# Kernel optimization log

Measured on AMD Instinct MI355X. Metric: run time of the kernel, lower is better.

Reference implementation:

```python
import jax, jax.numpy as jnp
import numpy as np

H, P, G, NS, K = 8, 64, 64, 64, 3          # heads, dim_head, slice_num, d_state, d_conv
D_INNER = H * P                            # 512
CONV_DIM = D_INNER + 2 * NS                # 640
D_IN_PROJ = 2 * D_INNER + 2 * NS + 2 * H   # 1168


def setup_inputs() -> dict:
    key = jax.random.key(0)
    ks = jax.random.split(key, 10)
    dim, Bsz, N = 256, 4, 8192
    s = 0.02
    return {
        "x": jax.random.normal(ks[0], (Bsz, N, dim), jnp.float32),
        "W_fx": jax.random.normal(ks[1], (D_INNER, dim), jnp.float32) * s,
        "b_fx": jnp.zeros((D_INNER,), jnp.float32),
        "W_x": jax.random.normal(ks[2], (D_INNER, dim), jnp.float32) * s,
        "b_x": jnp.zeros((D_INNER,), jnp.float32),
        "W_slice": jax.random.normal(ks[3], (G, P), jnp.float32) * s,
        "b_slice": jnp.zeros((G,), jnp.float32),
        "temperature": jnp.full((1, H, 1, 1), 0.5, jnp.float32),
        "hy_in_w": jax.random.normal(ks[4], (D_IN_PROJ, D_INNER), jnp.float32) * s,
        "hy_conv_w": jax.random.normal(ks[5], (CONV_DIM, K), jnp.float32) * s,
        "hy_conv_b": jnp.zeros((CONV_DIM,), jnp.float32),
        "hy_dt_bias": jnp.log(jnp.expm1(jnp.full((H,), 0.01, jnp.float32))),
        "hy_A_log": jnp.log(jnp.linspace(1.0, 16.0, H)).astype(jnp.float32),
        "hy_D": jnp.ones((H,), jnp.float32),
        "hy_fcD_w": jax.random.normal(ks[6], (H, D_INNER), jnp.float32) * s,
        "hy_norm_w": jnp.ones((D_INNER,), jnp.float32),
        "hy_out_w": jax.random.normal(ks[7], (D_INNER, D_INNER), jnp.float32) * s,
        "out_w": jax.random.normal(ks[8], (dim, D_INNER), jnp.float32) * s,
        "out_b": jnp.zeros((dim,), jnp.float32),
    }


def _hydra(u, in_w, conv_w, conv_b, dt_bias, A_log, Dp, fcD_w, norm_w, out_w):
    # Bidirectional Mamba2-style selective scan (Hydra, non mem-eff path).
    Bt, L, _ = u.shape
    zxbcdt = u @ in_w.T                                   # (B, L, 1168)
    z = zxbcdt[..., :D_INNER]
    xBC = zxbcdt[..., D_INNER:D_INNER + CONV_DIM]
    dt = zxbcdt[..., -2 * H:]
    # fwd dts for fwd copies, time-flipped bwd dts stacked along batch
    dt = jnp.concatenate([dt[..., :H], jnp.flip(dt[..., H:], axis=1)], axis=0)
    dt = jax.nn.softplus(dt + dt_bias)                    # (2B, L, H)
    # depthwise causal conv, kernel K, left pad K-1 then silu
    xp = jnp.pad(xBC, ((0, 0), (K - 1, 0), (0, 0)))
    xBC = sum(xp[:, k:k + L, :] * conv_w[:, k] for k in range(K)) + conv_b
    xBC = jax.nn.silu(xBC)
    x = xBC[..., :D_INNER]
    Bm = xBC[..., D_INNER:D_INNER + NS]
    Cm = xBC[..., D_INNER + NS:]
    x_og = x
    x2 = jnp.concatenate([x, jnp.flip(x, 1)], 0).reshape(2 * Bt, L, H, P)
    B2 = jnp.concatenate([Bm, jnp.flip(Bm, 1)], 0)        # (2B, L, NS)
    C2 = jnp.concatenate([Cm, jnp.flip(Cm, 1)], 0)
    dA = jnp.exp(dt * (-jnp.exp(A_log)))                  # (2B, L, H)
    dBx = jnp.einsum('blh,bln,blhp->blhpn', dt, B2, x2)   # (2B, L, H, P, NS)

    def step(h, inp):
        dA_t, dBx_t, C_t = inp
        h = h * dA_t[:, :, None, None] + dBx_t
        return h, jnp.einsum('bhpn,bn->bhp', h, C_t)

    h0 = jnp.zeros((2 * Bt, H, P, NS), u.dtype)
    _, ys = jax.lax.scan(step, h0, (dA.transpose(1, 0, 2), dBx.transpose(1, 0, 2, 3, 4), C2.transpose(1, 0, 2)))
    y = ys.transpose(1, 0, 2, 3).reshape(2 * Bt, L, D_INNER)
    y_fw, y_bw = y[:Bt], jnp.flip(y[Bt:], 1)
    # quasiseparable: strictly-lower (shift fwd) + strictly-upper (shift bwd) + diagonal
    y = jnp.pad(y_fw[:, :-1], ((0, 0), (1, 0), (0, 0))) + jnp.pad(y_bw[:, 1:], ((0, 0), (0, 1), (0, 0)))
    y = y + x_og * jnp.repeat(x_og @ fcD_w.T + Dp, P, axis=-1)
    # gated RMSNorm (gate before norm), then out projection
    yg = y * jax.nn.silu(z)
    yg = yg * jax.lax.rsqrt(jnp.mean(jnp.square(yg), -1, keepdims=True) + 1e-5) * norm_w
    return yg @ out_w.T


def reference(x, W_fx, b_fx, W_x, b_x, W_slice, b_slice, temperature,
              hy_in_w, hy_conv_w, hy_conv_b, hy_dt_bias, hy_A_log, hy_D,
              hy_fcD_w, hy_norm_w, hy_out_w, out_w, out_b):
    B, N, _ = x.shape
    fx = (x @ W_fx.T + b_fx).reshape(B, N, H, P).transpose(0, 2, 1, 3)   # (B,H,N,P)
    xm = (x @ W_x.T + b_x).reshape(B, N, H, P).transpose(0, 2, 1, 3)
    temp = jnp.maximum(temperature, 1e-6)
    sw = jax.nn.softmax((xm @ W_slice.T + b_slice) / temp, axis=-1)      # (B,H,N,G)
    snorm = sw.sum(2)                                                     # (B,H,G)
    st = jnp.einsum('bhnc,bhng->bhgc', fx, sw) / (snorm + 1e-5)[..., None]
    st = st.transpose(0, 2, 1, 3).reshape(B, G, D_INNER)                  # (B,G,512)
    ot = _hydra(st, hy_in_w, hy_conv_w, hy_conv_b, hy_dt_bias, hy_A_log, hy_D,
                hy_fcD_w, hy_norm_w, hy_out_w)
    ot = ot.reshape(B, G, H, P).transpose(0, 2, 1, 3)                     # (B,H,G,P)
    out = jnp.einsum('bhgc,bhng->bhnc', ot, sw).transpose(0, 2, 1, 3).reshape(B, N, D_INNER)
    return out @ out_w.T + out_b
```

## Files before the change

kernel.cpp:

```cpp
#include <hip/hip_runtime.h>
#include <hip/hip_bf16.h>
#include <cstdint>
#include <cstddef>

#define Hh 8
#define DIN 512
#define CONVD 640
#define DPROJ 1168
#define NTOK 8192
#define DIM 256

typedef __attribute__((ext_vector_type(8))) short short8;
typedef __attribute__((ext_vector_type(4))) float f32x4;

static __device__ __forceinline__ float sigmoidf_(float x) { return 1.f / (1.f + expf(-x)); }
static __device__ __forceinline__ unsigned short f2b(float f) {
  __hip_bfloat16 h = __float2bfloat16(f);
  return *(unsigned short*)&h;
}
static __device__ __forceinline__ float b2f(unsigned short u) {
  union { unsigned int i; float f; } cv; cv.i = ((unsigned int)u) << 16; return cv.f;
}
static __device__ __forceinline__ void gll16(const void* g, void* l) {
  __builtin_amdgcn_global_load_lds((const __attribute__((address_space(1))) void*)g,
                                   (__attribute__((address_space(3))) void*)l, 16, 0, 0);
}

__global__ __launch_bounds__(256) void k_cvt(
    const float* __restrict__ wfx, const float* __restrict__ wx, const float* __restrict__ outw,
    const float* __restrict__ inw, const float* __restrict__ how,
    const float* __restrict__ bfx, const float* __restrict__ bx,
    const float* __restrict__ x,
    unsigned short* __restrict__ wcat, unsigned short* __restrict__ outwb,
    unsigned short* __restrict__ inwb, unsigned short* __restrict__ howb,
    float* __restrict__ bcat, unsigned short* __restrict__ xb) {
  const int blk = blockIdx.x;
  if (blk < 4096) {
    const int e = (blk * 256 + threadIdx.x) * 8;
    float4 v0 = *(const float4*)(x + e);
    float4 v1 = *(const float4*)(x + e + 4);
    short8 o;
    o[0] = (short)f2b(v0.x); o[1] = (short)f2b(v0.y);
    o[2] = (short)f2b(v0.z); o[3] = (short)f2b(v0.w);
    o[4] = (short)f2b(v1.x); o[5] = (short)f2b(v1.y);
    o[6] = (short)f2b(v1.z); o[7] = (short)f2b(v1.w);
    *(short8*)(xb + e) = o;
    return;
  }
  const int e = ((blk - 4096) * 256 + threadIdx.x) * 4;
  if (e >= 1253376) {
    const int i = e - 1253376;
    float4 v;
    if (i < 512) v = *(const float4*)(bfx + i);
    else         v = *(const float4*)(bx + (i - 512));
    *(float4*)(bcat + i) = v;
    return;
  }
  const float* src; unsigned short* dst; int i;
  if (e < 131072)        { i = e;           src = wfx;  dst = wcat; }
  else if (e < 262144)   { i = e - 131072;  src = wx;   dst = wcat + 131072; }
  else if (e < 393216)   { i = e - 262144;  src = outw; dst = outwb; }
  else if (e < 991232)   { i = e - 393216;  src = inw;  dst = inwb; }
  else                   { i = e - 991232;  src = how;  dst = howb; }
  float4 v = *(const float4*)(src + i);
  ushort4 o;
  o.x = f2b(v.x); o.y = f2b(v.y); o.z = f2b(v.z); o.w = f2b(v.w);
  *(ushort4*)(dst + i) = o;
}

__global__ __launch_bounds__(256) void k_front(
    const unsigned short* __restrict__ xb, const unsigned short* __restrict__ wcat,
    const float* __restrict__ bcat, const float* __restrict__ Wslice,
    const float* __restrict__ bslice, const float* __restrict__ temperature,
    unsigned short* __restrict__ cb, unsigned short* __restrict__ swb) {
  __shared__ unsigned short lds[32768];
  const int tid = threadIdx.x;
  const int m0 = blockIdx.x * 128;
  const int n0 = blockIdx.y * 128;
  const int w = tid >> 6, lane = tid & 63;
  const int l15 = lane & 15, kq = lane >> 4;
  const int wm = (w & 1) * 64, wn = (w >> 1) * 64;
  float bs[4];
#pragma unroll
  for (int j = 0; j < 4; ++j) bs[j] = bcat[n0 + wn + j * 16 + l15];
  f32x4 acc[4][4];
#pragma unroll
  for (int i = 0; i < 4; ++i)
#pragma unroll
    for (int j = 0; j < 4; ++j) acc[i][j] = (f32x4){0.f, 0.f, 0.f, 0.f};

  auto stage = [&](int buf, int kt) {
    unsigned short* As = lds + buf * 8192;
    unsigned short* Bs = lds + 16384 + buf * 8192;
#pragma unroll
    for (int i = 0; i < 4; ++i) {
      const int c = tid + 256 * i;
      const int m = c >> 3, kb = c & 7;
      const int kbs = (kb ^ (m & 7)) * 8;
      gll16(&xb[(size_t)(m0 + m) * 256 + kt + kbs], &As[c * 8]);
      gll16(&wcat[(size_t)(n0 + m) * 256 + kt + kbs], &Bs[c * 8]);
    }
  };

  stage(0, 0);
  __syncthreads();
  int buf = 0;
  for (int t = 0; t < 4; ++t) {
    if (t < 3) stage(buf ^ 1, (t + 1) * 64);
    const unsigned short* As = lds + buf * 8192;
    const unsigned short* Bs = lds + 16384 + buf * 8192;
#pragma unroll
    for (int kw = 0; kw < 2; ++kw) {
      short8 af[4], bfr[4];
#pragma unroll
      for (int i = 0; i < 4; ++i) {
        const int rm = wm + i * 16 + l15;
        af[i]  = *(const short8*)&As[rm * 64 + ((kw * 32 + kq * 8) ^ ((rm & 7) << 3))];
        const int rn = wn + i * 16 + l15;
        bfr[i] = *(const short8*)&Bs[rn * 64 + ((kw * 32 + kq * 8) ^ ((rn & 7) << 3))];
      }
#pragma unroll
      for (int i = 0; i < 4; ++i)
#pragma unroll
        for (int j = 0; j < 4; ++j)
          acc[i][j] = __builtin_amdgcn_mfma_f32_16x16x32_bf16(af[i], bfr[j], acc[i][j], 0, 0, 0);
    }
    __syncthreads();
    buf ^= 1;
  }
  unsigned short* Cs = lds;
#pragma unroll
  for (int i = 0; i < 4; ++i)
#pragma unroll
    for (int j = 0; j < 4; ++j)
#pragma unroll
      for (int r = 0; r < 4; ++r) {
        const int m = wm + i * 16 + kq * 4 + r;
        const int n = wn + j * 16 + l15;
        Cs[m * 136 + n] = f2b(acc[i][j][r] + bs[j]);
      }
  __syncthreads();
  if (blockIdx.y < 4) {
#pragma unroll
    for (int it = 0; it < 8; ++it) {
      const int c = tid + 256 * it;
      const int m = c >> 4, seg = c & 15;
      *(short8*)&cb[(size_t)(m0 + m) * 512 + n0 + seg * 8] = *(const short8*)&Cs[m * 136 + seg * 8];
    }
    return;
  }
  const int h0 = (n0 - 512) >> 6;
  const int bidx = m0 >> 13, nb = m0 & (NTOK - 1);
  short8 sbfr[2][4];
#pragma unroll
  for (int kt = 0; kt < 2; ++kt)
#pragma unroll
    for (int j = 0; j < 4; ++j) {
      const float* wp = Wslice + (j * 16 + l15) * 64 + kt * 32 + kq * 8;
      short8 t;
#pragma unroll
      for (int u = 0; u < 8; ++u) t[u] = (short)f2b(wp[u]);
      sbfr[kt][j] = t;
    }
  float sbs[4];
#pragma unroll
  for (int j = 0; j < 4; ++j) sbs[j] = bslice[j * 16 + l15];
  f32x4 sacc[2][2][4];
#pragma unroll
  for (int hl = 0; hl < 2; ++hl)
#pragma unroll
    for (int i = 0; i < 2; ++i)
#pragma unroll
      for (int j = 0; j < 4; ++j) sacc[hl][i][j] = (f32x4){0.f, 0.f, 0.f, 0.f};
#pragma unroll
  for (int hl = 0; hl < 2; ++hl)
#pragma unroll
    for (int kt = 0; kt < 2; ++kt) {
      short8 af[2];
#pragma unroll
      for (int i = 0; i < 2; ++i)
        af[i] = *(const short8*)&Cs[(w * 32 + i * 16 + l15) * 136 + hl * 64 + kt * 32 + kq * 8];
#pragma unroll
      for (int i = 0; i < 2; ++i)
#pragma unroll
        for (int j = 0; j < 4; ++j)
          sacc[hl][i][j] = __builtin_amdgcn_mfma_f32_16x16x32_bf16(af[i], sbfr[kt][j], sacc[hl][i][j], 0, 0, 0);
    }
  __syncthreads();
#pragma unroll
  for (int hl = 0; hl < 2; ++hl) {
    const float invt = 1.f / fmaxf(temperature[h0 + hl], 1e-6f);
#pragma unroll
    for (int i = 0; i < 2; ++i)
#pragma unroll
      for (int r = 0; r < 4; ++r) {
        float v[4];
        float m = -1e30f;
#pragma unroll
        for (int j = 0; j < 4; ++j) { v[j] = (sacc[hl][i][j][r] + sbs[j]) * invt; m = fmaxf(m, v[j]); }
#pragma unroll
        for (int off = 8; off; off >>= 1) m = fmaxf(m, __shfl_xor(m, off));
        float s = 0.f;
#pragma unroll
        for (int j = 0; j < 4; ++j) { v[j] = expf(v[j] - m); s += v[j]; }
#pragma unroll
        for (int off = 8; off; off >>= 1) s += __shfl_xor(s, off);
        const float inv = 1.f / s;
        const int row = w * 32 + i * 16 + kq * 4 + r;
#pragma unroll
        for (int j = 0; j < 4; ++j) Cs[row * 136 + hl * 64 + j * 16 + l15] = f2b(v[j] * inv);
      }
  }
  __syncthreads();
#pragma unroll
  for (int it = 0; it < 8; ++it) {
    const int c = tid + 256 * it;
    const int head = c >> 10, row = (c >> 3) & 127, seg = c & 7;
    *(short8*)&swb[((size_t)(bidx * 8 + h0 + head) * NTOK + nb + row) * 64 + seg * 8] =
        *(const short8*)&Cs[row * 136 + head * 64 + seg * 8];
  }
}

__global__ __launch_bounds__(256) void k_st(
    const unsigned short* __restrict__ swb, const unsigned short* __restrict__ cb,
    float* __restrict__ st_part, float* __restrict__ sn_part) {
  __shared__ unsigned short swT[64][136];
  __shared__ unsigned short fxT[64][136];
  const int tid = threadIdx.x;
  const int bh = blockIdx.y;
  const int b = bh >> 3, h = bh & 7;
  const int nbase = blockIdx.x * 512;
  const int w = tid >> 6, lane = tid & 63;
  const int l15 = lane & 15, kq = lane >> 4;
  short8 ones;
#pragma unroll
  for (int u = 0; u < 8; ++u) ones[u] = (short)0x3F80;
  f32x4 acc[4], accO[4];
#pragma unroll
  for (int i = 0; i < 4; ++i) {
    acc[i] = (f32x4){0.f, 0.f, 0.f, 0.f};
    accO[i] = (f32x4){0.f, 0.f, 0.f, 0.f};
  }
  for (int nc = 0; nc < 4; ++nc) {
    const int n0 = nbase + nc * 128;
#pragma unroll
    for (int i = 0; i < 4; ++i) {
      const int c = tid + 256 * i, n = c >> 3, gc = c & 7;
      short8 sv = *(const short8*)&swb[((size_t)bh * NTOK + n0 + n) * 64 + gc * 8];
      short8 fv = *(const short8*)&cb[((size_t)(b * NTOK) + n0 + n) * 512 + h * 64 + gc * 8];
      const int csw = n ^ (gc << 4);
#pragma unroll
      for (int u = 0; u < 8; ++u) {
        swT[gc * 8 + u][csw] = (unsigned short)sv[u];
        fxT[gc * 8 + u][csw] = (unsigned short)fv[u];
      }
    }
    __syncthreads();
#pragma unroll
    for (int kw = 0; kw < 4; ++kw) {
      const int brow = w * 16 + l15;
      const short8 bfr = *(const short8*)&fxT[brow][(kw * 32 + kq * 8) ^ ((brow >> 3) << 4)];
#pragma unroll
      for (int mi = 0; mi < 4; ++mi) {
        const int arow = mi * 16 + l15;
        const short8 af = *(const short8*)&swT[arow][(kw * 32 + kq * 8) ^ ((arow >> 3) << 4)];
        acc[mi] = __builtin_amdgcn_mfma_f32_16x16x32_bf16(af, bfr, acc[mi], 0, 0, 0);
        if (w == 0)
          accO[mi] = __builtin_amdgcn_mfma_f32_16x16x32_bf16(af, ones, accO[mi], 0, 0, 0);
      }
    }
    __syncthreads();
  }
  float* stp = st_part + ((size_t)blockIdx.x * 32 + bh) * 4096;
#pragma unroll
  for (int mi = 0; mi < 4; ++mi)
#pragma unroll
    for (int r = 0; r < 4; ++r)
      stp[(mi * 16 + kq * 4 + r) * 64 + w * 16 + l15] = acc[mi][r];
  if (w == 0 && l15 == 0) {
    float* snp = sn_part + ((size_t)blockIdx.x * 32 + bh) * 64;
#pragma unroll
    for (int mi = 0; mi < 4; ++mi)
#pragma unroll
      for (int r = 0; r < 4; ++r)
        snp[mi * 16 + kq * 4 + r] = accO[mi][r];
  }
}

__global__ __launch_bounds__(256) void k_stnorm(
    const float* __restrict__ st_part, const float* __restrict__ sn_part,
    unsigned short* __restrict__ st2b) {
  const int idx = blockIdx.x * 256 + threadIdx.x;
  const int p = idx & 63, g = (idx >> 6) & 63, h = (idx >> 12) & 7, b = idx >> 15;
  const int bh = idx >> 12;
  const int gp = idx & 4095;
  float s = 0.f, sn = 0.f;
#pragma unroll
  for (int bx = 0; bx < 16; ++bx) {
    s  += st_part[((size_t)bx * 32 + bh) * 4096 + gp];
    sn += sn_part[((size_t)bx * 32 + bh) * 64 + g];
  }
  const float v = s / (sn + 1e-5f);
  st2b[(size_t)(b * 64 + g) * DIN + h * 64 + p] = f2b(v);
}

__global__ __launch_bounds__(256) void k_inproj(
    const unsigned short* __restrict__ st2b, const unsigned short* __restrict__ inwb,
    float* __restrict__ zx) {
  const int tid = threadIdx.x;
  const int m0 = blockIdx.x * 64;
  const int n0 = blockIdx.y * 64;
  const int w = tid >> 6, lane = tid & 63;
  const int l15 = lane & 15, kq = lane >> 4;
  f32x4 acc[4];
#pragma unroll
  for (int j = 0; j < 4; ++j) acc[j] = (f32x4){0.f, 0.f, 0.f, 0.f};
  const int arow = m0 + w * 16 + l15;
#pragma unroll
  for (int kc = 0; kc < 16; ++kc) {
    const short8 af = *(const short8*)&st2b[(size_t)arow * DIN + kc * 32 + kq * 8];
#pragma unroll
    for (int j = 0; j < 4; ++j) {
      int brow = n0 + j * 16 + l15;
      if (brow >= DPROJ) brow = 0;
      const short8 bfr = *(const short8*)&inwb[(size_t)brow * DIN + kc * 32 + kq * 8];
      acc[j] = __builtin_amdgcn_mfma_f32_16x16x32_bf16(af, bfr, acc[j], 0, 0, 0);
    }
  }
#pragma unroll
  for (int j = 0; j < 4; ++j)
#pragma unroll
    for (int r = 0; r < 4; ++r) {
      const int m = m0 + w * 16 + kq * 4 + r;
      const int c = n0 + j * 16 + l15;
      if (c < DPROJ) zx[(size_t)m * DPROJ + c] = acc[j][r];
    }
}

__global__ __launch_bounds__(256) void k_prep(
    const float* __restrict__ zx, const float* __restrict__ convw, const float* __restrict__ convb,
    const float* __restrict__ dtbias, const float* __restrict__ Alog,
    float* __restrict__ xbc, float* __restrict__ dt2, float* __restrict__ ldA2) {
  const int idx = blockIdx.x * 256 + threadIdx.x;
  const int NCONV = 4 * 64 * CONVD;
  if (idx < NCONV) {
    const int c = idx % CONVD;
    const int l = (idx / CONVD) & 63;
    const int b = idx / (CONVD * 64);
    float acc = convb[c];
#pragma unroll
    for (int k = 0; k < 3; ++k) {
      const int ls = l - 2 + k;
      if (ls >= 0) acc += zx[(size_t)(b * 64 + ls) * DPROJ + DIN + c] * convw[c * 3 + k];
    }
    xbc[idx] = acc * sigmoidf_(acc);
  } else if (idx < NCONV + 8 * 64 * 8) {
    const int j = idx - NCONV;
    const int h = j & 7, l = (j >> 3) & 63, bb = j >> 9;
    float raw;
    if (bb < 4) raw = zx[(size_t)(bb * 64 + l) * DPROJ + 1152 + h];
    else        raw = zx[(size_t)((bb - 4) * 64 + (63 - l)) * DPROJ + 1160 + h];
    const float d = raw + dtbias[h];
    const float sp = (d > 20.f) ? d : log1pf(expf(d));
    dt2[j] = sp;
    ldA2[j] = sp * -expf(Alog[h]);
  }
}

__global__ __launch_bounds__(256) void k_ssm(
    const float* __restrict__ xbc, const float* __restrict__ dt2, const float* __restrict__ ldA2,
    float* __restrict__ ys) {
  __shared__ unsigned short s_C[64][72];
  __shared__ unsigned short s_Bm[64][72];
  __shared__ unsigned short s_X[64][72];
  __shared__ unsigned short s_G[64][72];
  __shared__ float s_L[64];
  __shared__ float s_dt[64];
  const int blk = blockIdx.x;
  const int h = blk & 7, bb = blk >> 3;
  const int b = (bb < 4) ? bb : bb - 4;
  const bool rev = bb >= 4;
  const int tid = threadIdx.x;
  const int w = tid >> 6, lane = tid & 63;
  const int l15 = lane & 15, kq = lane >> 4;
  {
    const int l = tid >> 2, part = tid & 3;
    const int t = rev ? 63 - l : l;
    const float* src = xbc + (size_t)(b * 64 + l) * CONVD + DIN + part * 32;
#pragma unroll
    for (int u = 0; u < 32; u += 4) {
      float4 v = *(const float4*)(src + u);
      const int c = part * 32 + u;
      unsigned short* dst = (c < 64) ? &s_Bm[t][c] : &s_C[t][c - 64];
      dst[0] = f2b(v.x); dst[1] = f2b(v.y); dst[2] = f2b(v.z); dst[3] = f2b(v.w);
    }
    const float* xs = xbc + (size_t)(b * 64 + l) * CONVD + h * 64 + part * 16;
#pragma unroll
    for (int u = 0; u < 16; u += 4) {
      float4 v = *(const float4*)(xs + u);
      const int p = part * 16 + u;
      s_X[p + 0][t] = f2b(v.x); s_X[p + 1][t] = f2b(v.y);
      s_X[p + 2][t] = f2b(v.z); s_X[p + 3][t] = f2b(v.w);
    }
  }
  if (w == 0) {
    const float dtv = dt2[(bb * 64 + lane) * 8 + h];
    float ld = ldA2[(bb * 64 + lane) * 8 + h];
#pragma unroll
    for (int off = 1; off < 64; off <<= 1) {
      const float o = __shfl_up(ld, off);
      if (lane >= off) ld += o;
    }
    s_L[lane] = ld;
    s_dt[lane] = dtv;
  }
  __syncthreads();
  f32x4 accS[4];
#pragma unroll
  for (int i = 0; i < 4; ++i) accS[i] = (f32x4){0.f, 0.f, 0.f, 0.f};
#pragma unroll
  for (int kw = 0; kw < 2; ++kw) {
    const short8 bfr = *(const short8*)&s_Bm[w * 16 + l15][kw * 32 + kq * 8];
#pragma unroll
    for (int i = 0; i < 4; ++i) {
      const short8 af = *(const short8*)&s_C[i * 16 + l15][kw * 32 + kq * 8];
      accS[i] = __builtin_amdgcn_mfma_f32_16x16x32_bf16(af, bfr, accS[i], 0, 0, 0);
    }
  }
  const int s_idx = w * 16 + l15;
  const float Ls = s_L[s_idx];
  const float dts = s_dt[s_idx];
#pragma unroll
  for (int i = 0; i < 4; ++i)
#pragma unroll
    for (int r = 0; r < 4; ++r) {
      const int t = i * 16 + kq * 4 + r;
      const float g = (s_idx <= t) ? accS[i][r] * expf(s_L[t] - Ls) * dts : 0.f;
      s_G[t][s_idx] = f2b(g);
    }
  __syncthreads();
  f32x4 accY[4];
#pragma unroll
  for (int i = 0; i < 4; ++i) accY[i] = (f32x4){0.f, 0.f, 0.f, 0.f};
#pragma unroll
  for (int kw = 0; kw < 2; ++kw) {
    const short8 bfr = *(const short8*)&s_X[w * 16 + l15][kw * 32 + kq * 8];
#pragma unroll
    for (int i = 0; i < 4; ++i) {
      const short8 af = *(const short8*)&s_G[i * 16 + l15][kw * 32 + kq * 8];
      accY[i] = __builtin_amdgcn_mfma_f32_16x16x32_bf16(af, bfr, accY[i], 0, 0, 0);
    }
  }
#pragma unroll
  for (int i = 0; i < 4; ++i)
#pragma unroll
    for (int r = 0; r < 4; ++r) {
      const int t = i * 16 + kq * 4 + r;
      ys[(((size_t)(bb * 64 + t) * 8 + h) << 6) + w * 16 + l15] = accY[i][r];
    }
}

__global__ __launch_bounds__(256) void k_gate(
    const float* __restrict__ ys, const float* __restrict__ xbc, const float* __restrict__ zx,
    const float* __restrict__ fcdw, const float* __restrict__ Dp,
    const float* __restrict__ normw, unsigned short* __restrict__ ygb) {
  __shared__ float red[256][9];
  __shared__ float s_xfc[8];
  const int bl = blockIdx.x;
  const int b = bl >> 6, l = bl & 63;
  const int tid = threadIdx.x;
  const float xog0 = xbc[(size_t)bl * CONVD + tid];
  const float xog1 = xbc[(size_t)bl * CONVD + 256 + tid];
#pragma unroll
  for (int h = 0; h < 8; ++h)
    red[tid][h] = xog0 * fcdw[h * DIN + tid] + xog1 * fcdw[h * DIN + 256 + tid];
  __syncthreads();
  for (int s = 128; s > 0; s >>= 1) {
    if (tid < s) {
#pragma unroll
      for (int h = 0; h < 8; ++h) red[tid][h] += red[tid + s][h];
    }
    __syncthreads();
  }
  if (tid < 8) s_xfc[tid] = red[0][tid] + Dp[tid];
  __syncthreads();
  float ygv[2];
  float sumsq = 0.f;
#pragma unroll
  for (int ci = 0; ci < 2; ++ci) {
    const int c = tid + ci * 256;
    const int h = c >> 6, p = c & 63;
    float yv = 0.f;
    if (l >= 1)  yv += ys[(((size_t)(b * 64 + (l - 1)) * 8 + h) << 6) + p];
    if (l <= 62) yv += ys[(((size_t)((4 + b) * 64 + (62 - l)) * 8 + h) << 6) + p];
    const float xog = (ci == 0) ? xog0 : xog1;
    yv += xog * s_xfc[h];
    const float z = zx[(size_t)bl * DPROJ + c];
    const float g = yv * (z * sigmoidf_(z));
    ygv[ci] = g;
    sumsq += g * g;
  }
  red[tid][0] = sumsq;
  __syncthreads();
  for (int s = 128; s > 0; s >>= 1) {
    if (tid < s) red[tid][0] += red[tid + s][0];
    __syncthreads();
  }
  const float scale = 1.f / sqrtf(red[0][0] / 512.f + 1e-5f);
#pragma unroll
  for (int ci = 0; ci < 2; ++ci) {
    const int c = tid + ci * 256;
    ygb[(size_t)bl * DIN + c] = f2b(ygv[ci] * scale * normw[c]);
  }
}

__global__ __launch_bounds__(256) void k_oproj(
    const unsigned short* __restrict__ ygb, const unsigned short* __restrict__ howb,
    unsigned short* __restrict__ otT) {
  __shared__ unsigned short Cs[64][72];
  const int tid = threadIdx.x;
  const int b = blockIdx.x;
  const int h = blockIdx.y;
  const int m0 = b * 64, n0 = h * 64;
  const int w = tid >> 6, lane = tid & 63;
  const int l15 = lane & 15, kq = lane >> 4;
  f32x4 acc[4];
#pragma unroll
  for (int j = 0; j < 4; ++j) acc[j] = (f32x4){0.f, 0.f, 0.f, 0.f};
  const int arow = m0 + w * 16 + l15;
#pragma unroll
  for (int kc = 0; kc < 16; ++kc) {
    const short8 af = *(const short8*)&ygb[(size_t)arow * DIN + kc * 32 + kq * 8];
#pragma unroll
    for (int j = 0; j < 4; ++j) {
      const int brow = n0 + j * 16 + l15;
      const short8 bfr = *(const short8*)&howb[(size_t)brow * DIN + kc * 32 + kq * 8];
      acc[j] = __builtin_amdgcn_mfma_f32_16x16x32_bf16(af, bfr, acc[j], 0, 0, 0);
    }
  }
#pragma unroll
  for (int j = 0; j < 4; ++j)
#pragma unroll
    for (int r = 0; r < 4; ++r) {
      const int g = w * 16 + kq * 4 + r;
      const int p = j * 16 + l15;
      Cs[p][g] = f2b(acc[j][r]);
    }
  __syncthreads();
#pragma unroll
  for (int it = 0; it < 2; ++it) {
    const int c = tid + 256 * it;
    const int p = c >> 3, seg = c & 7;
    *(short8*)&otT[(((size_t)(b * 8 + h) * 64 + p) << 6) + seg * 8] = *(const short8*)&Cs[p][seg * 8];
  }
}

__global__ __launch_bounds__(256) void k_mixfinal(
    const unsigned short* __restrict__ swb, const unsigned short* __restrict__ otT,
    const unsigned short* __restrict__ outwb, const float* __restrict__ outb,
    float* __restrict__ out) {
  __shared__ unsigned short lm[33280];
  const int blk = blockIdx.x;
  const int b = blk >> 7;
  const int t0 = (blk & 127) * 64;
  const int tid = threadIdx.x;
  const int w = tid >> 6, lane = tid & 63;
  const int l15 = lane & 15, kq = lane >> 4;
#pragma unroll
  for (int hh = 0; hh < 2; ++hh) {
    const int h = w * 2 + hh;
    const int bh = b * 8 + h;
    f32x4 acc[4][4];
#pragma unroll
    for (int i = 0; i < 4; ++i)
#pragma unroll
      for (int j = 0; j < 4; ++j) acc[i][j] = (f32x4){0.f, 0.f, 0.f, 0.f};
#pragma unroll
    for (int kt = 0; kt < 2; ++kt) {
      short8 af[4], bfr[4];
#pragma unroll
      for (int i = 0; i < 4; ++i) {
        af[i]  = *(const short8*)&swb[((size_t)bh * NTOK + t0 + i * 16 + l15) * 64 + kt * 32 + kq * 8];
        bfr[i] = *(const short8*)&otT[(((size_t)bh * 64 + i * 16 + l15) << 6) + kt * 32 + kq * 8];
      }
#pragma unroll
      for (int i = 0; i < 4; ++i)
#pragma unroll
        for (int j = 0; j < 4; ++j)
          acc[i][j] = __builtin_amdgcn_mfma_f32_16x16x32_bf16(af[i], bfr[j], acc[i][j], 0, 0, 0);
    }
#pragma unroll
    for (int i = 0; i < 4; ++i)
#pragma unroll
      for (int j = 0; j < 4; ++j)
#pragma unroll
        for (int r = 0; r < 4; ++r)
          lm[(i * 16 + kq * 4 + r) * 520 + h * 64 + j * 16 + l15] = f2b(acc[i][j][r]);
  }
  __syncthreads();
  float ob[4];
#pragma unroll
  for (int j = 0; j < 4; ++j) ob[j] = outb[w * 64 + j * 16 + l15];
  f32x4 facc[4][4];
#pragma unroll
  for (int i = 0; i < 4; ++i)
#pragma unroll
    for (int j = 0; j < 4; ++j) facc[i][j] = (f32x4){0.f, 0.f, 0.f, 0.f};
#pragma unroll
  for (int kt = 0; kt < 16; ++kt) {
    short8 af[4], bfr[4];
#pragma unroll
    for (int i = 0; i < 4; ++i) {
      af[i]  = *(const short8*)&lm[(i * 16 + l15) * 520 + kt * 32 + kq * 8];
      bfr[i] = *(const short8*)&outwb[(size_t)(w * 64 + i * 16 + l15) * 512 + kt * 32 + kq * 8];
    }
#pragma unroll
    for (int i = 0; i < 4; ++i)
#pragma unroll
      for (int j = 0; j < 4; ++j)
        facc[i][j] = __builtin_amdgcn_mfma_f32_16x16x32_bf16(af[i], bfr[j], facc[i][j], 0, 0, 0);
  }
  __syncthreads();
  float* lf = (float*)lm;
#pragma unroll
  for (int i = 0; i < 4; ++i)
#pragma unroll
    for (int j = 0; j < 4; ++j)
#pragma unroll
      for (int r = 0; r < 4; ++r)
        lf[(i * 16 + kq * 4 + r) * 260 + w * 64 + j * 16 + l15] = facc[i][j][r] + ob[j];
  __syncthreads();
#pragma unroll
  for (int it = 0; it < 16; ++it) {
    const int c = tid + 256 * it;
    const int row = c >> 6, seg = c & 63;
    *(float4*)&out[((size_t)(b * NTOK + t0 + row)) * 256 + seg * 4] =
        *(const float4*)&lf[row * 260 + seg * 4];
  }
}

extern "C" void kernel_launch(void* const* d_in, const int* in_sizes, int n_in,
                              void* d_out, int out_size, void* d_ws, size_t ws_size,
                              hipStream_t stream) {
  const float* x      = (const float*)d_in[0];
  const float* Wfx    = (const float*)d_in[1];
  const float* bfx    = (const float*)d_in[2];
  const float* Wx     = (const float*)d_in[3];
  const float* bx     = (const float*)d_in[4];
  const float* Wslice = (const float*)d_in[5];
  const float* bslice = (const float*)d_in[6];
  const float* temp   = (const float*)d_in[7];
  const float* inw    = (const float*)d_in[8];
  const float* convw  = (const float*)d_in[9];
  const float* convb  = (const float*)d_in[10];
  const float* dtbias = (const float*)d_in[11];
  const float* Alog   = (const float*)d_in[12];
  const float* Dp     = (const float*)d_in[13];
  const float* fcdw   = (const float*)d_in[14];
  const float* normw  = (const float*)d_in[15];
  const float* how    = (const float*)d_in[16];
  const float* outw   = (const float*)d_in[17];
  const float* outb   = (const float*)d_in[18];

  unsigned short* us = (unsigned short*)d_ws;
  unsigned short* cb     = us;
  unsigned short* swb    = cb + 16777216;
  unsigned short* wcatb  = swb + 16777216;
  unsigned short* outwbf = wcatb + 262144;
  unsigned short* otTb   = outwbf + 131072;
  unsigned short* inwb   = otTb + 131072;
  unsigned short* howb   = inwb + 598016;
  unsigned short* st2b   = howb + 262144;
  unsigned short* ygbb   = st2b + 131072;
  unsigned short* xbb    = ygbb + 131072;
  float* fbase = (float*)(xbb + 8388608);
  float* bcat    = fbase;
  float* st_part = bcat + 1024;
  float* sn_part = st_part + 2097152;
  float* zx      = sn_part + 32768;
  float* xbc     = zx + 299008;
  float* dt2     = xbc + 163840;
  float* ldA2    = dt2 + 4096;
  float* ysb     = ldA2 + 4096;

  k_cvt     <<<dim3(5321),    256, 0, stream>>>(Wfx, Wx, outw, inw, how, bfx, bx, x,
                                                wcatb, outwbf, inwb, howb, bcat, xbb);
  k_front   <<<dim3(256, 8),  256, 0, stream>>>(xbb, wcatb, bcat, Wslice, bslice, temp, cb, swb);
  k_st      <<<dim3(16, 32),  256, 0, stream>>>(swb, cb, st_part, sn_part);
  k_stnorm  <<<dim3(512),     256, 0, stream>>>(st_part, sn_part, st2b);
  k_inproj  <<<dim3(4, 19),   256, 0, stream>>>(st2b, inwb, zx);
  k_prep    <<<dim3(656),     256, 0, stream>>>(zx, convw, convb, dtbias, Alog, xbc, dt2, ldA2);
  k_ssm     <<<dim3(64),      256, 0, stream>>>(xbc, dt2, ldA2, ysb);
  k_gate    <<<dim3(256),     256, 0, stream>>>(ysb, xbc, zx, fcdw, Dp, normw, ygbb);
  k_oproj   <<<dim3(4, 8),    256, 0, stream>>>(ygbb, howb, otTb);
  k_mixfinal<<<dim3(512),     256, 0, stream>>>(swb, otTb, outwbf, outb, (float*)d_out);
}
```

Before: 249.9 us.

## Fuse slice-token reduction into front GEMM with per-head fx/xm tiles

The front GEMM now computes, per block, the fx and xm columns for a single head. It fuses the softmax slice weights and the sw^T·fx slice-token reduction directly into that kernel. This eliminates the fx intermediate buffer (cb) round trip through global memory and the separate k_st launch. Partial sums are accumulated with float atomics into zeroed partial buffers, which adds a memset and atomic traffic as a trade-off.

```diff
diff --git a/kernel.cpp b/kernel.cpp
--- a/kernel.cpp
+++ b/kernel.cpp
@@ -72,17 +72,19 @@
     const unsigned short* __restrict__ xb, const unsigned short* __restrict__ wcat,
     const float* __restrict__ bcat, const float* __restrict__ Wslice,
     const float* __restrict__ bslice, const float* __restrict__ temperature,
-    unsigned short* __restrict__ cb, unsigned short* __restrict__ swb) {
-  __shared__ unsigned short lds[32768];
+    unsigned short* __restrict__ swb, float* __restrict__ st_part,
+    float* __restrict__ sn_part) {
+  __shared__ unsigned short lds[34816];
   const int tid = threadIdx.x;
   const int m0 = blockIdx.x * 128;
-  const int n0 = blockIdx.y * 128;
+  const int h = blockIdx.y;
   const int w = tid >> 6, lane = tid & 63;
   const int l15 = lane & 15, kq = lane >> 4;
   const int wm = (w & 1) * 64, wn = (w >> 1) * 64;
+  const int bbase = (wn == 0) ? h * 64 : 512 + h * 64;
   float bs[4];
 #pragma unroll
-  for (int j = 0; j < 4; ++j) bs[j] = bcat[n0 + wn + j * 16 + l15];
+  for (int j = 0; j < 4; ++j) bs[j] = bcat[bbase + j * 16 + l15];
   f32x4 acc[4][4];
 #pragma unroll
   for (int i = 0; i < 4; ++i)
@@ -98,7 +100,8 @@
       const int m = c >> 3, kb = c & 7;
       const int kbs = (kb ^ (m & 7)) * 8;
       gll16(&xb[(size_t)(m0 + m) * 256 + kt + kbs], &As[c * 8]);
-      gll16(&wcat[(size_t)(n0 + m) * 256 + kt + kbs], &Bs[c * 8]);
+      const int wr = (m < 64) ? (h * 64 + m) : (448 + h * 64 + m);
+      gll16(&wcat[(size_t)wr * 256 + kt + kbs], &Bs[c * 8]);
     }
   };
 
@@ -140,17 +143,7 @@
         Cs[m * 136 + n] = f2b(acc[i][j][r] + bs[j]);
       }
   __syncthreads();
-  if (blockIdx.y < 4) {
-#pragma unroll
-    for (int it = 0; it < 8; ++it) {
-      const int c = tid + 256 * it;
-      const int m = c >> 4, seg = c & 15;
-      *(short8*)&cb[(size_t)(m0 + m) * 512 + n0 + seg * 8] = *(const short8*)&Cs[m * 136 + seg * 8];
-    }
-    return;
-  }
-  const int h0 = (n0 - 512) >> 6;
-  const int bidx = m0 >> 13, nb = m0 & (NTOK - 1);
+
   short8 sbfr[2][4];
 #pragma unroll
   for (int kt = 0; kt < 2; ++kt)
@@ -165,125 +158,103 @@
   float sbs[4];
 #pragma unroll
   for (int j = 0; j < 4; ++j) sbs[j] = bslice[j * 16 + l15];
-  f32x4 sacc[2][2][4];
-#pragma unroll
-  for (int hl = 0; hl < 2; ++hl)
+  f32x4 sacc[2][4];
+#pragma unroll
+  for (int i = 0; i < 2; ++i)
+#pragma unroll
+    for (int j = 0; j < 4; ++j) sacc[i][j] = (f32x4){0.f, 0.f, 0.f, 0.f};
+#pragma unroll
+  for (int kt = 0; kt < 2; ++kt) {
+    short8 af[2];
 #pragma unroll
     for (int i = 0; i < 2; ++i)
-#pragma unroll
-      for (int j = 0; j < 4; ++j) sacc[hl][i][j] = (f32x4){0.f, 0.f, 0.f, 0.f};
-#pragma unroll
-  for (int hl = 0; hl < 2; ++hl)
-#pragma unroll
-    for (int kt = 0; kt < 2; ++kt) {
-      short8 af[2];
-#pragma unroll
-      for (int i = 0; i < 2; ++i)
-        af[i] = *(const short8*)&Cs[(w * 32 + i * 16 + l15) * 136 + hl * 64 + kt * 32 + kq * 8];
-#pragma unroll
-      for (int i = 0; i < 2; ++i)
-#pragma unroll
-        for (int j = 0; j < 4; ++j)
-          sacc[hl][i][j] = __builtin_amdgcn_mfma_f32_16x16x32_bf16(af[i], sbfr[kt][j], sacc[hl][i][j], 0, 0, 0);
-    }
-  __syncthreads();
-#pragma unroll
-  for (int hl = 0; hl < 2; ++hl) {
-    const float invt = 1.f / fmaxf(temperature[h0 + hl], 1e-6f);
+      af[i] = *(const short8*)&Cs[(w * 32 + i * 16 + l15) * 136 + 64 + kt * 32 + kq * 8];
 #pragma unroll
     for (int i = 0; i < 2; ++i)
 #pragma unroll
-      for (int r = 0; r < 4; ++r) {
-        float v[4];
-        float m = -1e30f;
-#pragma unroll
-        for (int j = 0; j < 4; ++j) { v[j] = (sacc[hl][i][j][r] + sbs[j]) * invt; m = fmaxf(m, v[j]); }
-#pragma unroll
-        for (int off = 8; off; off >>= 1) m = fmaxf(m, __shfl_xor(m, off));
-        float s = 0.f;
-#pragma unroll
-        for (int j = 0; j < 4; ++j) { v[j] = expf(v[j] - m); s += v[j]; }
-#pragma unroll
-        for (int off = 8; off; off >>= 1) s += __shfl_xor(s, off);
-        const float inv = 1.f / s;
-        const int row = w * 32 + i * 16 + kq * 4 + r;
-#pragma unroll
-        for (int j = 0; j < 4; ++j) Cs[row * 136 + hl * 64 + j * 16 + l15] = f2b(v[j] * inv);
+      for (int j = 0; j < 4; ++j)
+        sacc[i][j] = __builtin_amdgcn_mfma_f32_16x16x32_bf16(af[i], sbfr[kt][j], sacc[i][j], 0, 0, 0);
+  }
+  __syncthreads();
+
+  unsigned short* swT = lds + 17408;
+  unsigned short* fxT = lds + 26112;
+  const float invt = 1.f / fmaxf(temperature[h], 1e-6f);
+#pragma unroll
+  for (int i = 0; i < 2; ++i)
+#pragma unroll
+    for (int r = 0; r < 4; ++r) {
+      float v[4];
+      float m = -1e30f;
+#pragma unroll
+      for (int j = 0; j < 4; ++j) { v[j] = (sacc[i][j][r] + sbs[j]) * invt; m = fmaxf(m, v[j]); }
+#pragma unroll
+      for (int off = 8; off; off >>= 1) m = fmaxf(m, __shfl_xor(m, off));
+      float s = 0.f;
+#pragma unroll
+      for (int j = 0; j < 4; ++j) { v[j] = expf(v[j] - m); s += v[j]; }
+#pragma unroll
+      for (int off = 8; off; off >>= 1) s += __shfl_xor(s, off);
+      const float inv = 1.f / s;
+      const int row = w * 32 + i * 16 + kq * 4 + r;
+#pragma unroll
+      for (int j = 0; j < 4; ++j) {
+        const unsigned short us = f2b(v[j] * inv);
+        Cs[row * 136 + 64 + j * 16 + l15] = us;
+        swT[(j * 16 + l15) * 136 + row] = us;
       }
-  }
-  __syncthreads();
-#pragma unroll
-  for (int it = 0; it < 8; ++it) {
+    }
+#pragma unroll
+  for (int i = 0; i < 4; ++i) {
+    const int c = tid + 256 * i;
+    const int n = c >> 3, pc = c & 7;
+    const short8 t = *(const short8*)&Cs[n * 136 + pc * 8];
+#pragma unroll
+    for (int u = 0; u < 8; ++u) fxT[(pc * 8 + u) * 136 + n] = (unsigned short)t[u];
+  }
+  __syncthreads();
+
+  short8 ones;
+#pragma unroll
+  for (int u = 0; u < 8; ++u) ones[u] = (short)0x3F80;
+  f32x4 st_acc[4];
+  f32x4 accO = (f32x4){0.f, 0.f, 0.f, 0.f};
+#pragma unroll
+  for (int j = 0; j < 4; ++j) st_acc[j] = (f32x4){0.f, 0.f, 0.f, 0.f};
+#pragma unroll
+  for (int kt = 0; kt < 4; ++kt) {
+    const short8 af = *(const short8*)&swT[(w * 16 + l15) * 136 + kt * 32 + kq * 8];
+#pragma unroll
+    for (int j = 0; j < 4; ++j) {
+      const short8 bf = *(const short8*)&fxT[(j * 16 + l15) * 136 + kt * 32 + kq * 8];
+      st_acc[j] = __builtin_amdgcn_mfma_f32_16x16x32_bf16(af, bf, st_acc[j], 0, 0, 0);
+    }
+    accO = __builtin_amdgcn_mfma_f32_16x16x32_bf16(af, ones, accO, 0, 0, 0);
+  }
+
+  const int bidx = m0 >> 13, nb = m0 & (NTOK - 1);
+  const int bh = bidx * 8 + h;
+#pragma unroll
+  for (int it = 0; it < 4; ++it) {
     const int c = tid + 256 * it;
-    const int head = c >> 10, row = (c >> 3) & 127, seg = c & 7;
-    *(short8*)&swb[((size_t)(bidx * 8 + h0 + head) * NTOK + nb + row) * 64 + seg * 8] =
-        *(const short8*)&Cs[row * 136 + head * 64 + seg * 8];
-  }
-}
-
-__global__ __launch_bounds__(256) void k_st(
-    const unsigned short* __restrict__ swb, const unsigned short* __restrict__ cb,
-    float* __restrict__ st_part, float* __restrict__ sn_part) {
-  __shared__ unsigned short swT[64][136];
-  __shared__ unsigned short fxT[64][136];
-  const int tid = threadIdx.x;
-  const int bh = blockIdx.y;
-  const int b = bh >> 3, h = bh & 7;
-  const int nbase = blockIdx.x * 512;
-  const int w = tid >> 6, lane = tid & 63;
-  const int l15 = lane & 15, kq = lane >> 4;
-  short8 ones;
-#pragma unroll
-  for (int u = 0; u < 8; ++u) ones[u] = (short)0x3F80;
-  f32x4 acc[4], accO[4];
-#pragma unroll
-  for (int i = 0; i < 4; ++i) {
-    acc[i] = (f32x4){0.f, 0.f, 0.f, 0.f};
-    accO[i] = (f32x4){0.f, 0.f, 0.f, 0.f};
-  }
-  for (int nc = 0; nc < 4; ++nc) {
-    const int n0 = nbase + nc * 128;
-#pragma unroll
-    for (int i = 0; i < 4; ++i) {
-      const int c = tid + 256 * i, n = c >> 3, gc = c & 7;
-      short8 sv = *(const short8*)&swb[((size_t)bh * NTOK + n0 + n) * 64 + gc * 8];
-      short8 fv = *(const short8*)&cb[((size_t)(b * NTOK) + n0 + n) * 512 + h * 64 + gc * 8];
-      const int csw = n ^ (gc << 4);
-#pragma unroll
-      for (int u = 0; u < 8; ++u) {
-        swT[gc * 8 + u][csw] = (unsigned short)sv[u];
-        fxT[gc * 8 + u][csw] = (unsigned short)fv[u];
-      }
-    }
-    __syncthreads();
-#pragma unroll
-    for (int kw = 0; kw < 4; ++kw) {
-      const int brow = w * 16 + l15;
-      const short8 bfr = *(const short8*)&fxT[brow][(kw * 32 + kq * 8) ^ ((brow >> 3) << 4)];
-#pragma unroll
-      for (int mi = 0; mi < 4; ++mi) {
-        const int arow = mi * 16 + l15;
-        const short8 af = *(const short8*)&swT[arow][(kw * 32 + kq * 8) ^ ((arow >> 3) << 4)];
-        acc[mi] = __builtin_amdgcn_mfma_f32_16x16x32_bf16(af, bfr, acc[mi], 0, 0, 0);
-        if (w == 0)
-          accO[mi] = __builtin_amdgcn_mfma_f32_16x16x32_bf16(af, ones, accO[mi], 0, 0, 0);
-      }
-    }
-    __syncthreads();
-  }
-  float* stp = st_part + ((size_t)blockIdx.x * 32 + bh) * 4096;
-#pragma unroll
-  for (int mi = 0; mi < 4; ++mi)
+    const int n = c >> 3, seg = c & 7;
+    *(short8*)&swb[((size_t)bh * NTOK + nb + n) * 64 + seg * 8] =
+        *(const short8*)&Cs[n * 136 + 64 + seg * 8];
+  }
+
+  const int chunk = blockIdx.x & 15;
+  float* stp = st_part + ((size_t)(chunk * 32 + bh)) * 4096;
+  const int g = w * 16 + kq * 4;
+#pragma unroll
+  for (int j = 0; j < 4; ++j)
 #pragma unroll
     for (int r = 0; r < 4; ++r)
-      stp[(mi * 16 + kq * 4 + r) * 64 + w * 16 + l15] = acc[mi][r];
-  if (w == 0 && l15 == 0) {
-    float* snp = sn_part + ((size_t)blockIdx.x * 32 + bh) * 64;
-#pragma unroll
-    for (int mi = 0; mi < 4; ++mi)
-#pragma unroll
-      for (int r = 0; r < 4; ++r)
-        snp[mi * 16 + kq * 4 + r] = accO[mi][r];
+      atomicAdd(&stp[(g + r) * 64 + j * 16 + l15], st_acc[j][r]);
+  if (l15 == 0) {
+    float* snp = sn_part + ((size_t)(chunk * 32 + bh)) * 64;
+#pragma unroll
+    for (int r = 0; r < 4; ++r)
+      atomicAdd(&snp[g + r], accO[r]);
   }
 }
 
@@ -663,8 +634,7 @@
   const float* outb   = (const float*)d_in[18];
 
   unsigned short* us = (unsigned short*)d_ws;
-  unsigned short* cb     = us;
-  unsigned short* swb    = cb + 16777216;
+  unsigned short* swb    = us;
   unsigned short* wcatb  = swb + 16777216;
   unsigned short* outwbf = wcatb + 262144;
   unsigned short* otTb   = outwbf + 131072;
@@ -683,10 +653,12 @@
   float* ldA2    = dt2 + 4096;
   float* ysb     = ldA2 + 4096;
 
+  hipMemsetAsync(st_part, 0, (2097152 + 32768) * sizeof(float), stream);
+
   k_cvt     <<<dim3(5321),    256, 0, stream>>>(Wfx, Wx, outw, inw, how, bfx, bx, x,
                                                 wcatb, outwbf, inwb, howb, bcat, xbb);
-  k_front   <<<dim3(256, 8),  256, 0, stream>>>(xbb, wcatb, bcat, Wslice, bslice, temp, cb, swb);
-  k_st      <<<dim3(16, 32),  256, 0, stream>>>(swb, cb, st_part, sn_part);
+  k_front   <<<dim3(256, 8),  256, 0, stream>>>(xbb, wcatb, bcat, Wslice, bslice, temp,
+                                                swb, st_part, sn_part);
   k_stnorm  <<<dim3(512),     256, 0, stream>>>(st_part, sn_part, st2b);
   k_inproj  <<<dim3(4, 19),   256, 0, stream>>>(st2b, inwb, zx);
   k_prep    <<<dim3(656),     256, 0, stream>>>(zx, convw, convb, dtbias, Alog, xbc, dt2, ldA2);
```

Result: slower. 266.2 us (+6.5%).
